# Optimization experiments

Hardware: AMD Instinct MI355X
Metric: run time of the kernel (lower is better)

## Reference

```python
import jax, jax.numpy as jnp
import numpy as np


def setup_inputs() -> dict:
    key = jax.random.key(0)
    k1, k2, k3, k4, k5 = jax.random.split(key, 5)
    B, T, D, L = 8, 512, 512, 24
    V = 50000
    x = jax.random.normal(k1, (B, T, D), dtype=jnp.float32) * 0.1
    node_vecs = jax.random.normal(k2, (V - 1, D), dtype=jnp.float32) * 0.05
    paths = jax.random.randint(k3, (B, T, L), 0, V - 1, dtype=jnp.int32)
    codes = jax.random.randint(k4, (B, T, L), 0, 2, dtype=jnp.int32)
    mask = jax.random.randint(k5, (B, T, L), 0, 2, dtype=jnp.int32)
    return {"x": x, "node_vecs": node_vecs, "paths": paths, "codes": codes, "mask": mask}


def reference(x, node_vecs, paths, codes, mask):
    # x: [B, T, D] input word vectors
    # node_vecs: [V-1, D] Huffman internal-node parameters
    # paths: [B, T, L] internal-node indices along each target word's path
    # codes: [B, T, L] Huffman bits (0/1); mask: [B, T, L] valid-depth mask
    B = x.shape[0]
    path_vecs = node_vecs[paths]                     # [B, T, L, D] gather
    logits = jnp.einsum('btd,btld->btl', x, path_vecs)
    signs = 1.0 - 2.0 * codes.astype(x.dtype)        # bit 0 -> +1, bit 1 -> -1
    # per-node -log sigmoid(sign * logit); sum over path, words; avg over sequences
    node_nll = -jax.nn.log_sigmoid(signs * logits) * mask.astype(x.dtype)
    return jnp.sum(node_nll) / B
```

## Files before the change

### kernel.cpp

```cpp
#include <hip/hip_runtime.h>

#define BB 8
#define TT 512
#define DD 512
#define LL 24

__global__ void hs_zero_out(float* out) { out[0] = 0.0f; }

__global__ __launch_bounds__(256) void hs_kernel(
    const float* __restrict__ x,
    const float* __restrict__ node_vecs,
    const int* __restrict__ paths,
    const int* __restrict__ codes,
    const int* __restrict__ mask,
    float* __restrict__ out)
{
    const int bt   = blockIdx.x;
    const int tid  = threadIdx.x;
    const int lane = tid & 63;
    const int wave = tid >> 6;

    __shared__ float xs[DD];
    __shared__ float wsum[4];

    const float4* xg  = (const float4*)(x + (size_t)bt * DD);
    float4*       xs4 = (float4*)xs;
    if (tid < DD / 4) xs4[tid] = xg[tid];
    __syncthreads();

    const int base = bt * LL;
    float local = 0.0f;

    for (int l = wave; l < LL; l += 4) {
        const int m = mask[base + l];
        if (m == 0) continue;
        const int idx = paths[base + l];
        const int c   = codes[base + l];

        const float4* nv = (const float4*)(node_vecs + (size_t)idx * DD);
        float4 a0 = nv[lane];
        float4 a1 = nv[lane + 64];
        float4 b0 = xs4[lane];
        float4 b1 = xs4[lane + 64];

        float dot = a0.x * b0.x + a0.y * b0.y + a0.z * b0.z + a0.w * b0.w
                  + a1.x * b1.x + a1.y * b1.y + a1.z * b1.z + a1.w * b1.w;

        #pragma unroll
        for (int off = 32; off >= 1; off >>= 1)
            dot += __shfl_xor(dot, off, 64);

        const float sign = 1.0f - 2.0f * (float)c;
        const float z    = -sign * dot;
        const float nll  = fmaxf(z, 0.0f) + log1pf(expf(-fabsf(z)));
        local += nll;
    }

    if (lane == 0) wsum[wave] = local;
    __syncthreads();
    if (tid == 0) {
        const float s = wsum[0] + wsum[1] + wsum[2] + wsum[3];
        atomicAdd(out, s * (1.0f / (float)BB));
    }
}

extern "C" void kernel_launch(void* const* d_in, const int* in_sizes, int n_in,
                              void* d_out, int out_size, void* d_ws, size_t ws_size,
                              hipStream_t stream) {
    const float* x         = (const float*)d_in[0];
    const float* node_vecs = (const float*)d_in[1];
    const int*   paths     = (const int*)d_in[2];
    const int*   codes     = (const int*)d_in[3];
    const int*   mask      = (const int*)d_in[4];
    float*       out       = (float*)d_out;

    hs_zero_out<<<1, 1, 0, stream>>>(out);
    hs_kernel<<<BB * TT, 256, 0, stream>>>(x, node_vecs, paths, codes, mask, out);
}
```

Measured before the change: 196.7 us.

## Batch gather loads per wave and prefetch path metadata into LDS

Each wave now handles six contiguous path depths, issuing all six node-vector gathers before any reduction. This raises memory-level parallelism and interleaves the shuffle reductions across independent dots. Path, code and mask indices are loaded cooperatively into shared memory alongside x. Masked entries still load row 0 (a cached dummy) instead of being skipped, and register use rises.

Result: no change. 194.3 us (-1.2%).

```diff
diff --git a/kernel.cpp b/kernel.cpp
--- a/kernel.cpp
+++ b/kernel.cpp
@@ -4,6 +4,7 @@
 #define TT 512
 #define DD 512
 #define LL 24
+#define LPW 6
 
 __global__ void hs_zero_out(float* out) { out[0] = 0.0f; }
 
@@ -21,47 +22,66 @@
     const int wave = tid >> 6;
 
     __shared__ float xs[DD];
+    __shared__ int   mpaths[LL];
+    __shared__ int   mcodes[LL];
+    __shared__ int   mmask[LL];
     __shared__ float wsum[4];
 
     const float4* xg  = (const float4*)(x + (size_t)bt * DD);
     float4*       xs4 = (float4*)xs;
-    if (tid < DD / 4) xs4[tid] = xg[tid];
+    const int base = bt * LL;
+    if (tid < DD / 4)                      xs4[tid]          = xg[tid];
+    else if (tid >= 128 && tid < 128 + LL) mpaths[tid - 128] = paths[base + tid - 128];
+    else if (tid >= 160 && tid < 160 + LL) mcodes[tid - 160] = codes[base + tid - 160];
+    else if (tid >= 192 && tid < 192 + LL) mmask[tid - 192]  = mask[base + tid - 192];
     __syncthreads();
 
-    const int base = bt * LL;
+    const int l0 = wave * LPW;
+
+    const float4 b0 = xs4[lane];
+    const float4 b1 = xs4[lane + 64];
+
+    int    msk[LPW], cod[LPW];
+    float4 a0[LPW], a1[LPW];
+
+    #pragma unroll
+    for (int j = 0; j < LPW; ++j) {
+        const int l = l0 + j;
+        msk[j] = mmask[l];
+        cod[j] = mcodes[l];
+        const int idx = msk[j] ? mpaths[l] : 0;
+        const float4* nv = (const float4*)(node_vecs + (size_t)idx * DD);
+        a0[j] = nv[lane];
+        a1[j] = nv[lane + 64];
+    }
+
+    float dot[LPW];
+    #pragma unroll
+    for (int j = 0; j < LPW; ++j) {
+        dot[j] = a0[j].x * b0.x + a0[j].y * b0.y + a0[j].z * b0.z + a0[j].w * b0.w
+               + a1[j].x * b1.x + a1[j].y * b1.y + a1[j].z * b1.z + a1[j].w * b1.w;
+    }
+
+    #pragma unroll
+    for (int off = 32; off >= 1; off >>= 1) {
+        #pragma unroll
+        for (int j = 0; j < LPW; ++j)
+            dot[j] += __shfl_xor(dot[j], off, 64);
+    }
+
     float local = 0.0f;
-
-    for (int l = wave; l < LL; l += 4) {
-        const int m = mask[base + l];
-        if (m == 0) continue;
-        const int idx = paths[base + l];
-        const int c   = codes[base + l];
-
-        const float4* nv = (const float4*)(node_vecs + (size_t)idx * DD);
-        float4 a0 = nv[lane];
-        float4 a1 = nv[lane + 64];
-        float4 b0 = xs4[lane];
-        float4 b1 = xs4[lane + 64];
-
-        float dot = a0.x * b0.x + a0.y * b0.y + a0.z * b0.z + a0.w * b0.w
-                  + a1.x * b1.x + a1.y * b1.y + a1.z * b1.z + a1.w * b1.w;
-
-        #pragma unroll
-        for (int off = 32; off >= 1; off >>= 1)
-            dot += __shfl_xor(dot, off, 64);
-
-        const float sign = 1.0f - 2.0f * (float)c;
-        const float z    = -sign * dot;
+    #pragma unroll
+    for (int j = 0; j < LPW; ++j) {
+        const float sign = 1.0f - 2.0f * (float)cod[j];
+        const float z    = -sign * dot[j];
         const float nll  = fmaxf(z, 0.0f) + log1pf(expf(-fabsf(z)));
-        local += nll;
+        local += msk[j] ? nll : 0.0f;
     }
 
     if (lane == 0) wsum[wave] = local;
     __syncthreads();
-    if (tid == 0) {
-        const float s = wsum[0] + wsum[1] + wsum[2] + wsum[3];
-        atomicAdd(out, s * (1.0f / (float)BB));
-    }
+    if (tid == 0)
+        atomicAdd(out, (wsum[0] + wsum[1] + wsum[2] + wsum[3]) * (1.0f / (float)BB));
 }
 
 extern "C" void kernel_launch(void* const* d_in, const int* in_sizes, int n_in,
```
